# Kernel tuning notes

Measured on AMD Instinct MI355X. Metric: run time of the kernel, lower is better.

## Reference

```python
import jax, jax.numpy as jnp
import numpy as np

B, T, I, H = 1024, 2048, 12, 512


def setup_inputs() -> dict:
    key = jax.random.key(0)
    k1, k2, k3, k4 = jax.random.split(key, 4)
    s = 1.0 / np.sqrt(H)
    return {
        "history": jax.random.normal(k1, (B, T, I), dtype=jnp.float32),
        "w_ih": jax.random.normal(k2, (3 * H, I), dtype=jnp.float32) * s,
        "w_hh": jax.random.normal(k3, (3 * H, H), dtype=jnp.float32) * s,
        "w_out": jax.random.normal(k4, (2, H), dtype=jnp.float32) * s,
        "b_out": jnp.zeros((2,), dtype=jnp.float32),
    }


def reference(history, w_ih, w_hh, w_out, b_out):
    # GRUCell recurrence over T steps with per-step linear head (torch GRUCell math, bias=False)
    xs = jnp.transpose(history, (1, 0, 2))  # [T, B, I]
    h0 = jnp.zeros((history.shape[0], H), dtype=history.dtype)

    def step(h, x_t):
        gi = x_t @ w_ih.T            # [B, 3H]
        gh = h @ w_hh.T              # [B, 3H]
        i_r, i_z, i_n = jnp.split(gi, 3, axis=-1)
        h_r, h_z, h_n = jnp.split(gh, 3, axis=-1)
        r = jax.nn.sigmoid(i_r + h_r)
        z = jax.nn.sigmoid(i_z + h_z)
        n = jnp.tanh(i_n + r * h_n)
        h_new = (1.0 - z) * n + z * h
        logit = h_new @ w_out.T + b_out  # [B, 2]
        return h_new, logit

    h_final, logits = jax.lax.scan(step, h0, xs)
    return jnp.transpose(logits, (1, 0, 2)), h_final  # ([B, T, 2], [B, H])
```

## Files before the change

kernel.cpp:

```cpp
#include <hip/hip_runtime.h>
#include <stdint.h>


#define NB 256
#define NT 256
#define TB 1024
#define TT 2048
#define II 12
#define HH 512
#define NCL 32
#define GBLK 8
#define ROWS 32

#define HTILE_B (ROWS * HH * 2)
#define HBUF_B  ((size_t)NCL * HTILE_B)
#define BAR_OFF ((size_t)2 * HBUF_B)
#define WS_USED (BAR_OFF + (size_t)NCL * 128)

#define LDSB (ROWS * 1024)

#define GAS __attribute__((address_space(1)))
#define LAS __attribute__((address_space(3)))

typedef _Float16 half8 __attribute__((ext_vector_type(8)));
typedef float    f32x4 __attribute__((ext_vector_type(4)));

static __device__ __forceinline__ float fast_sigmoid(float x) {
  float e = exp2f(-1.44269504f * x);
  return __builtin_amdgcn_rcpf(1.0f + e);
}
static __device__ __forceinline__ float fast_tanh(float x) {
  float e = exp2f(2.88539008f * x);
  return 1.0f - 2.0f * __builtin_amdgcn_rcpf(1.0f + e);
}

static __device__ __forceinline__ void wait_flags32(unsigned* f, unsigned tgt,
                                                    int* dead) {
  const int l = threadIdx.x & 63;
  long spin = 0;
  for (;;) {
    unsigned v = __hip_atomic_load(f + (l & 31), __ATOMIC_RELAXED,
                                   __HIP_MEMORY_SCOPE_AGENT);
    if (__all(v >= tgt)) break;
    if (++spin > (1L << 24)) { *dead = 1; break; }
  }
}

__global__ void __launch_bounds__(NT, 1)
gru_persistent(const float* __restrict__ hist,
               const float* __restrict__ w_ih,
               const float* __restrict__ w_hh,
               const float* __restrict__ w_out,
               const float* __restrict__ b_out,
               float* __restrict__ out,
               uint8_t* __restrict__ ws)
{
  extern __shared__ char smem[];
  char* ldsA = smem;
  const int bid = blockIdx.x;
  const int c   = bid & 31;
  const int g   = bid >> 5;
  const int tid = threadIdx.x;
  const int w   = tid >> 6;
  const int l   = tid & 63;
  const int l15 = l & 15;
  const int l4  = l >> 4;
  const int crb = c * ROWS;
  unsigned* F = (unsigned*)(ws + BAR_OFF) + (size_t)c * 32;
  const int myflag = g * 4 + w;

  const int col0 = g * 64 + w * 16;
  const int pcol = col0 + l15;

  half8 wr[16], wz[16], wn[16];
#pragma unroll
  for (int ks = 0; ks < 16; ++ks) {
    const size_t Rr = (size_t)(0 * HH + col0 + l15) * HH + ks * 32 + l4 * 8;
    const size_t Rz = (size_t)(1 * HH + col0 + l15) * HH + ks * 32 + l4 * 8;
    const size_t Rn = (size_t)(2 * HH + col0 + l15) * HH + ks * 32 + l4 * 8;
#pragma unroll
    for (int i = 0; i < 8; ++i) {
      wr[ks][i] = (_Float16)w_hh[Rr + i];
      wz[ks][i] = (_Float16)w_hh[Rz + i];
      wn[ks][i] = (_Float16)w_hh[Rn + i];
    }
  }

  half8 wih[3];
#pragma unroll
  for (int gt = 0; gt < 3; ++gt) {
    const int R = gt * HH + col0 + l15;
#pragma unroll
    for (int i = 0; i < 8; ++i) {
      const int k = l4 * 8 + i;
      wih[gt][i] = (_Float16)((k < II) ? w_ih[R * II + k] : 0.0f);
    }
  }

  const int lr = g * 4 + w;
  const int jj = (l >> 4) & 1;
  float wor[32];
#pragma unroll
  for (int i = 0; i < 32; ++i) wor[i] = w_out[jj * HH + l15 * 32 + i];
  const float bo = b_out[jj];

  float hprev[2][4];
#pragma unroll
  for (int mt = 0; mt < 2; ++mt)
#pragma unroll
    for (int q = 0; q < 4; ++q) hprev[mt][q] = 0.0f;

  int deadlock = 0;

  f32x4 xn0[2], xn1[2];
#pragma unroll
  for (int mt = 0; mt < 2; ++mt) {
    xn0[mt] = (f32x4){0.f, 0.f, 0.f, 0.f};
    xn1[mt] = (f32x4){0.f, 0.f, 0.f, 0.f};
    const float* xp = hist + (size_t)(crb + mt * 16 + l15) * (TT * II);
    if (l4 == 0)      { xn0[mt] = *(const f32x4*)xp; xn1[mt] = *(const f32x4*)(xp + 4); }
    else if (l4 == 1) { xn0[mt] = *(const f32x4*)(xp + 8); }
  }

  for (int t = 0; t < TT; ++t) {
    const uint8_t* hsrc = ws + ((t & 1) ? HBUF_B : 0) + (size_t)c * HTILE_B;
    uint8_t*       hdst = ws + ((t & 1) ? 0 : HBUF_B) + (size_t)c * HTILE_B;

    if (t > 0) wait_flags32(F, (unsigned)t, &deadlock);
    __builtin_amdgcn_sched_barrier(0);

#pragma unroll
    for (int it = 0; it < 8; ++it)
      __builtin_amdgcn_global_load_lds(
          (const GAS uint32_t*)(hsrc + it * 4096 + tid * 16),
          (LAS uint32_t*)(ldsA + it * 4096 + tid * 16), 16, 0, 17);
    __builtin_amdgcn_sched_barrier(0);

    half8 ax[2];
#pragma unroll
    for (int mt = 0; mt < 2; ++mt)
#pragma unroll
      for (int i = 0; i < 4; ++i) {
        ax[mt][i]     = (_Float16)xn0[mt][i];
        ax[mt][4 + i] = (_Float16)xn1[mt][i];
      }
    {
      const int tx = (t + 1 < TT) ? (t + 1) : 0;
#pragma unroll
      for (int mt = 0; mt < 2; ++mt) {
        const float* xp = hist + (size_t)(crb + mt * 16 + l15) * (TT * II) + (size_t)tx * II;
        if (l4 == 0)      { xn0[mt] = *(const f32x4*)xp; xn1[mt] = *(const f32x4*)(xp + 4); }
        else if (l4 == 1) { xn0[mt] = *(const f32x4*)(xp + 8); }
      }
    }
    __builtin_amdgcn_sched_barrier(0);

    asm volatile("s_waitcnt vmcnt(10)" ::: "memory");
    __builtin_amdgcn_s_barrier();
    __builtin_amdgcn_sched_barrier(0);

    f32x4 acc0 = (f32x4){0.f, 0.f, 0.f, 0.f};
    f32x4 acc1 = acc0, acc2 = acc0;
    f32x4 accin = __builtin_amdgcn_mfma_f32_16x16x32_f16(ax[0], wih[2],
                    (f32x4){0.f, 0.f, 0.f, 0.f}, 0, 0, 0);
    acc0 = __builtin_amdgcn_mfma_f32_16x16x32_f16(ax[0], wih[0], acc0, 0, 0, 0);
    acc1 = __builtin_amdgcn_mfma_f32_16x16x32_f16(ax[0], wih[1], acc1, 0, 0, 0);
#pragma unroll
    for (int ks = 0; ks < 16; ++ks) {
      const int ko = (ks * 64 + l4 * 16) ^ (l15 << 4);
      half8 a = *(const half8*)(ldsA + l15 * 1024 + ko);
      acc0 = __builtin_amdgcn_mfma_f32_16x16x32_f16(a, wr[ks], acc0, 0, 0, 0);
      acc1 = __builtin_amdgcn_mfma_f32_16x16x32_f16(a, wz[ks], acc1, 0, 0, 0);
      acc2 = __builtin_amdgcn_mfma_f32_16x16x32_f16(a, wn[ks], acc2, 0, 0, 0);
    }

    if (t > 0 && lr < 16) {
      float s = 0.0f;
#pragma unroll
      for (int c8 = 0; c8 < 4; ++c8) {
        half8 hv = *(const half8*)(ldsA + lr * 1024 +
                                   ((l15 * 64 + c8 * 16) ^ ((lr & 15) << 4)));
#pragma unroll
        for (int i = 0; i < 8; ++i) s += (float)hv[i] * wor[c8 * 8 + i];
      }
#pragma unroll
      for (int off = 1; off < 16; off <<= 1) s += __shfl_xor(s, off);
      if (l15 == 0 && l < 32) out[((size_t)(crb + lr) * TT + (t - 1)) * 2 + jj] = s + bo;
    }

#pragma unroll
    for (int q = 0; q < 4; ++q) {
      const int m = l4 * 4 + q;
      const float r  = fast_sigmoid(acc0[q]);
      const float z  = fast_sigmoid(acc1[q]);
      const float n  = fast_tanh(accin[q] + r * acc2[q]);
      const float hn = (1.0f - z) * n + z * hprev[0][q];
      hprev[0][q] = hn;
      __hip_atomic_store(
          (unsigned short*)(hdst + m * 1024 + ((pcol * 2) ^ ((m & 15) << 4))),
          __builtin_bit_cast(unsigned short, (_Float16)hn),
          __ATOMIC_RELAXED, __HIP_MEMORY_SCOPE_AGENT);
    }
    __builtin_amdgcn_sched_barrier(0);

    asm volatile("s_waitcnt vmcnt(10)" ::: "memory");
    __builtin_amdgcn_s_barrier();
    __builtin_amdgcn_sched_barrier(0);

    acc0 = (f32x4){0.f, 0.f, 0.f, 0.f};
    acc1 = acc0; acc2 = acc0;
    accin = __builtin_amdgcn_mfma_f32_16x16x32_f16(ax[1], wih[2],
              (f32x4){0.f, 0.f, 0.f, 0.f}, 0, 0, 0);
    acc0 = __builtin_amdgcn_mfma_f32_16x16x32_f16(ax[1], wih[0], acc0, 0, 0, 0);
    acc1 = __builtin_amdgcn_mfma_f32_16x16x32_f16(ax[1], wih[1], acc1, 0, 0, 0);
#pragma unroll
    for (int ks = 0; ks < 16; ++ks) {
      const int ko = (ks * 64 + l4 * 16) ^ (l15 << 4);
      half8 a = *(const half8*)(ldsA + (16 + l15) * 1024 + ko);
      acc0 = __builtin_amdgcn_mfma_f32_16x16x32_f16(a, wr[ks], acc0, 0, 0, 0);
      acc1 = __builtin_amdgcn_mfma_f32_16x16x32_f16(a, wz[ks], acc1, 0, 0, 0);
      acc2 = __builtin_amdgcn_mfma_f32_16x16x32_f16(a, wn[ks], acc2, 0, 0, 0);
    }

    if (t > 0 && lr >= 16) {
      float s = 0.0f;
#pragma unroll
      for (int c8 = 0; c8 < 4; ++c8) {
        half8 hv = *(const half8*)(ldsA + lr * 1024 +
                                   ((l15 * 64 + c8 * 16) ^ ((lr & 15) << 4)));
#pragma unroll
        for (int i = 0; i < 8; ++i) s += (float)hv[i] * wor[c8 * 8 + i];
      }
#pragma unroll
      for (int off = 1; off < 16; off <<= 1) s += __shfl_xor(s, off);
      if (l15 == 0 && l < 32) out[((size_t)(crb + lr) * TT + (t - 1)) * 2 + jj] = s + bo;
    }

#pragma unroll
    for (int q = 0; q < 4; ++q) {
      const int m = 16 + l4 * 4 + q;
      const float r  = fast_sigmoid(acc0[q]);
      const float z  = fast_sigmoid(acc1[q]);
      const float n  = fast_tanh(accin[q] + r * acc2[q]);
      const float hn = (1.0f - z) * n + z * hprev[1][q];
      hprev[1][q] = hn;
      __hip_atomic_store(
          (unsigned short*)(hdst + m * 1024 + ((pcol * 2) ^ ((m & 15) << 4))),
          __builtin_bit_cast(unsigned short, (_Float16)hn),
          __ATOMIC_RELAXED, __HIP_MEMORY_SCOPE_AGENT);
    }
    __builtin_amdgcn_sched_barrier(0);

    asm volatile("s_waitcnt vmcnt(0)" ::: "memory");
    __builtin_amdgcn_sched_barrier(0);
    if (l == 0)
      __hip_atomic_store(F + myflag, (unsigned)(t + 1), __ATOMIC_RELAXED,
                         __HIP_MEMORY_SCOPE_AGENT);
  }

  wait_flags32(F, (unsigned)TT, &deadlock);
  {
    const uint8_t* hsrc = ws + ((TT & 1) ? HBUF_B : 0) + (size_t)c * HTILE_B;
#pragma unroll
    for (int it = 0; it < 8; ++it)
      __builtin_amdgcn_global_load_lds(
          (const GAS uint32_t*)(hsrc + it * 4096 + tid * 16),
          (LAS uint32_t*)(ldsA + it * 4096 + tid * 16), 16, 0, 17);
    asm volatile("s_waitcnt vmcnt(0)" ::: "memory");
    __builtin_amdgcn_s_barrier();

    float s = 0.0f;
#pragma unroll
    for (int c8 = 0; c8 < 4; ++c8) {
      half8 hv = *(const half8*)(ldsA + lr * 1024 +
                                 ((l15 * 64 + c8 * 16) ^ ((lr & 15) << 4)));
#pragma unroll
      for (int i = 0; i < 8; ++i) s += (float)hv[i] * wor[c8 * 8 + i];
    }
#pragma unroll
    for (int off = 1; off < 16; off <<= 1) s += __shfl_xor(s, off);
    if (l15 == 0 && l < 32) out[((size_t)(crb + lr) * TT + (TT - 1)) * 2 + jj] = s + bo;
  }

#pragma unroll
  for (int mt = 0; mt < 2; ++mt)
#pragma unroll
    for (int q = 0; q < 4; ++q) {
      const int m = mt * 16 + l4 * 4 + q;
      out[(size_t)TB * TT * 2 + (size_t)(crb + m) * HH + pcol] = hprev[mt][q];
    }
}

extern "C" void kernel_launch(void* const* d_in, const int* in_sizes, int n_in,
                              void* d_out, int out_size, void* d_ws, size_t ws_size,
                              hipStream_t stream) {
  (void)in_sizes; (void)n_in; (void)out_size;
  if (ws_size < WS_USED) return;

  const float* hist  = (const float*)d_in[0];
  const float* w_ih  = (const float*)d_in[1];
  const float* w_hh  = (const float*)d_in[2];
  const float* w_out = (const float*)d_in[3];
  const float* b_out = (const float*)d_in[4];
  float* out = (float*)d_out;
  uint8_t* ws = (uint8_t*)d_ws;

  hipMemsetAsync(d_ws, 0, WS_USED, stream);

  void* args[] = {(void*)&hist, (void*)&w_ih, (void*)&w_hh, (void*)&w_out,
                  (void*)&b_out, (void*)&out, (void*)&ws};
  hipError_t e = hipLaunchCooperativeKernel((const void*)gru_persistent,
                                            dim3(NB), dim3(NT), args,
                                            (unsigned)LDSB, stream);
  if (e != hipSuccess) {
    gru_persistent<<<dim3(NB), dim3(NT), LDSB, stream>>>(
        hist, w_ih, w_hh, w_out, b_out, out, ws);
  }
}
```

Measured before the change: 8.872 ms.

## Use per-block step flags and issue both row-tile MFMA chains back to back

Each block now publishes one progress flag per step, after a block-wide barrier, instead of one flag per wavefront. Waiters therefore poll 8 flags instead of 32. The two 16-row halves of the hidden-state matmul are now issued consecutively behind a single mid-step barrier, and the gate math and output head for both halves follow afterwards, so the per-half sync and head phases are merged. This cuts polling traffic and gives the MFMA pipe more independent work, at the cost of an extra block barrier per step and higher register pressure from holding two accumulator sets.

```diff
diff --git a/kernel.cpp b/kernel.cpp
--- a/kernel.cpp
+++ b/kernel.cpp
@@ -34,12 +34,12 @@
   return 1.0f - 2.0f * __builtin_amdgcn_rcpf(1.0f + e);
 }
 
-static __device__ __forceinline__ void wait_flags32(unsigned* f, unsigned tgt,
-                                                    int* dead) {
+static __device__ __forceinline__ void wait_flags8(unsigned* f, unsigned tgt,
+                                                   int* dead) {
   const int l = threadIdx.x & 63;
   long spin = 0;
   for (;;) {
-    unsigned v = __hip_atomic_load(f + (l & 31), __ATOMIC_RELAXED,
+    unsigned v = __hip_atomic_load(f + (l & 7), __ATOMIC_RELAXED,
                                    __HIP_MEMORY_SCOPE_AGENT);
     if (__all(v >= tgt)) break;
     if (++spin > (1L << 24)) { *dead = 1; break; }
@@ -66,8 +66,7 @@
   const int l15 = l & 15;
   const int l4  = l >> 4;
   const int crb = c * ROWS;
-  unsigned* F = (unsigned*)(ws + BAR_OFF) + (size_t)c * 32;
-  const int myflag = g * 4 + w;
+  unsigned* flags = (unsigned*)(ws + BAR_OFF) + c * 32;
 
   const int col0 = g * 64 + w * 16;
   const int pcol = col0 + l15;
@@ -97,7 +96,6 @@
     }
   }
 
-  const int lr = g * 4 + w;
   const int jj = (l >> 4) & 1;
   float wor[32];
 #pragma unroll
@@ -110,6 +108,7 @@
 #pragma unroll
     for (int q = 0; q < 4; ++q) hprev[mt][q] = 0.0f;
 
+  const int lr = (g * 4 + w) & 31;
   int deadlock = 0;
 
   f32x4 xn0[2], xn1[2];
@@ -126,8 +125,7 @@
     const uint8_t* hsrc = ws + ((t & 1) ? HBUF_B : 0) + (size_t)c * HTILE_B;
     uint8_t*       hdst = ws + ((t & 1) ? 0 : HBUF_B) + (size_t)c * HTILE_B;
 
-    if (t > 0) wait_flags32(F, (unsigned)t, &deadlock);
-    __builtin_amdgcn_sched_barrier(0);
+    if (t > 0) wait_flags8(flags, (unsigned)t, &deadlock);
 
 #pragma unroll
     for (int it = 0; it < 8; ++it)
@@ -173,19 +171,25 @@
       acc1 = __builtin_amdgcn_mfma_f32_16x16x32_f16(a, wz[ks], acc1, 0, 0, 0);
       acc2 = __builtin_amdgcn_mfma_f32_16x16x32_f16(a, wn[ks], acc2, 0, 0, 0);
     }
-
-    if (t > 0 && lr < 16) {
-      float s = 0.0f;
-#pragma unroll
-      for (int c8 = 0; c8 < 4; ++c8) {
-        half8 hv = *(const half8*)(ldsA + lr * 1024 +
-                                   ((l15 * 64 + c8 * 16) ^ ((lr & 15) << 4)));
-#pragma unroll
-        for (int i = 0; i < 8; ++i) s += (float)hv[i] * wor[c8 * 8 + i];
-      }
-#pragma unroll
-      for (int off = 1; off < 16; off <<= 1) s += __shfl_xor(s, off);
-      if (l15 == 0 && l < 32) out[((size_t)(crb + lr) * TT + (t - 1)) * 2 + jj] = s + bo;
+    __builtin_amdgcn_sched_barrier(0);
+
+    asm volatile("s_waitcnt vmcnt(6)" ::: "memory");
+    __builtin_amdgcn_s_barrier();
+    __builtin_amdgcn_sched_barrier(0);
+
+    f32x4 b0 = (f32x4){0.f, 0.f, 0.f, 0.f};
+    f32x4 b1 = b0, b2 = b0;
+    f32x4 bin = __builtin_amdgcn_mfma_f32_16x16x32_f16(ax[1], wih[2],
+                  (f32x4){0.f, 0.f, 0.f, 0.f}, 0, 0, 0);
+    b0 = __builtin_amdgcn_mfma_f32_16x16x32_f16(ax[1], wih[0], b0, 0, 0, 0);
+    b1 = __builtin_amdgcn_mfma_f32_16x16x32_f16(ax[1], wih[1], b1, 0, 0, 0);
+#pragma unroll
+    for (int ks = 0; ks < 16; ++ks) {
+      const int ko = (ks * 64 + l4 * 16) ^ (l15 << 4);
+      half8 a = *(const half8*)(ldsA + (16 + l15) * 1024 + ko);
+      b0 = __builtin_amdgcn_mfma_f32_16x16x32_f16(a, wr[ks], b0, 0, 0, 0);
+      b1 = __builtin_amdgcn_mfma_f32_16x16x32_f16(a, wz[ks], b1, 0, 0, 0);
+      b2 = __builtin_amdgcn_mfma_f32_16x16x32_f16(a, wn[ks], b2, 0, 0, 0);
     }
 
 #pragma unroll
@@ -201,28 +205,8 @@
           __builtin_bit_cast(unsigned short, (_Float16)hn),
           __ATOMIC_RELAXED, __HIP_MEMORY_SCOPE_AGENT);
     }
-    __builtin_amdgcn_sched_barrier(0);
-
-    asm volatile("s_waitcnt vmcnt(10)" ::: "memory");
-    __builtin_amdgcn_s_barrier();
-    __builtin_amdgcn_sched_barrier(0);
-
-    acc0 = (f32x4){0.f, 0.f, 0.f, 0.f};
-    acc1 = acc0; acc2 = acc0;
-    accin = __builtin_amdgcn_mfma_f32_16x16x32_f16(ax[1], wih[2],
-              (f32x4){0.f, 0.f, 0.f, 0.f}, 0, 0, 0);
-    acc0 = __builtin_amdgcn_mfma_f32_16x16x32_f16(ax[1], wih[0], acc0, 0, 0, 0);
-    acc1 = __builtin_amdgcn_mfma_f32_16x16x32_f16(ax[1], wih[1], acc1, 0, 0, 0);
-#pragma unroll
-    for (int ks = 0; ks < 16; ++ks) {
-      const int ko = (ks * 64 + l4 * 16) ^ (l15 << 4);
-      half8 a = *(const half8*)(ldsA + (16 + l15) * 1024 + ko);
-      acc0 = __builtin_amdgcn_mfma_f32_16x16x32_f16(a, wr[ks], acc0, 0, 0, 0);
-      acc1 = __builtin_amdgcn_mfma_f32_16x16x32_f16(a, wz[ks], acc1, 0, 0, 0);
-      acc2 = __builtin_amdgcn_mfma_f32_16x16x32_f16(a, wn[ks], acc2, 0, 0, 0);
-    }
-
-    if (t > 0 && lr >= 16) {
+
+    if (t > 0) {
       float s = 0.0f;
 #pragma unroll
       for (int c8 = 0; c8 < 4; ++c8) {
@@ -239,9 +223,9 @@
 #pragma unroll
     for (int q = 0; q < 4; ++q) {
       const int m = 16 + l4 * 4 + q;
-      const float r  = fast_sigmoid(acc0[q]);
-      const float z  = fast_sigmoid(acc1[q]);
-      const float n  = fast_tanh(accin[q] + r * acc2[q]);
+      const float r  = fast_sigmoid(b0[q]);
+      const float z  = fast_sigmoid(b1[q]);
+      const float n  = fast_tanh(bin[q] + r * b2[q]);
       const float hn = (1.0f - z) * n + z * hprev[1][q];
       hprev[1][q] = hn;
       __hip_atomic_store(
@@ -252,13 +236,13 @@
     __builtin_amdgcn_sched_barrier(0);
 
     asm volatile("s_waitcnt vmcnt(0)" ::: "memory");
-    __builtin_amdgcn_sched_barrier(0);
-    if (l == 0)
-      __hip_atomic_store(F + myflag, (unsigned)(t + 1), __ATOMIC_RELAXED,
+    __builtin_amdgcn_s_barrier();
+    if (tid == 0)
+      __hip_atomic_store(flags + g, (unsigned)(t + 1), __ATOMIC_RELAXED,
                          __HIP_MEMORY_SCOPE_AGENT);
   }
 
-  wait_flags32(F, (unsigned)TT, &deadlock);
+  wait_flags8(flags, (unsigned)TT, &deadlock);
   {
     const uint8_t* hsrc = ws + ((TT & 1) ? HBUF_B : 0) + (size_t)c * HTILE_B;
 #pragma unroll
```

Result: faster. 7.939 ms (-10.5%).
